# Performance work log

Hardware: AMD Instinct MI355X
Metric: run time of the kernel (lower is better)

Reference implementation:

```python
import jax, jax.numpy as jnp
import numpy as np

# --- Bark-band constants (from init_kwargs: bark_num=25, fs=32000, win_len=1024) ---
WIDTHS = np.array([3, 3, 3, 3, 4, 4, 4, 5, 5, 6, 7, 8, 9, 10, 12, 14, 18, 22, 29, 35, 42, 58, 80, 128])
NB = 24              # bark_num - 1 bands
F = 512              # win_len // 2 frequency bins (WIDTHS sums to 512)
FS = 32000
WIN = 1024
SEG = np.repeat(np.arange(NB), WIDTHS)          # [F] bin -> band id (0-based)
MASK = np.zeros((F, NB), dtype=np.float32)
MASK[np.arange(F), SEG] = 1.0                   # one-hot band membership [F, NB]
K = WIDTHS.astype(np.float32)                   # band widths k_i
# absolute threshold of hearing (tq) per bin, f = (bin+1)*fs/win_len
_f = (np.arange(F) + 1.0) * FS / WIN
TQ = (3.64 * (_f / 1000 + 1e-6) ** (-0.8)
      - 6.5 * np.exp(-0.6 * (_f / 1000 - 3.3) ** 2)
      + 1e-3 * (_f / 1000) ** 4).astype(np.float32)

B, T = 32, 1200


def setup_inputs() -> dict:
    key = jax.random.key(0)
    k1, k2, k3, k4 = jax.random.split(key, 4)
    return {
        "log_magnitude": jax.random.normal(k1, (B, T, F), dtype=jnp.float32),
        "real": jax.random.normal(k2, (B, T, F), dtype=jnp.float32),
        "imag": jax.random.normal(k3, (B, T, F), dtype=jnp.float32),
        "spread_function": jax.random.uniform(k4, (NB, NB), dtype=jnp.float32),
    }


def reference(log_magnitude, real, imag, spread_function):
    eps = 1e-8
    spec = jnp.exp(jnp.clip(log_magnitude, -1000.0, 10.0))          # [B,T,F], > 0
    dt = spec.dtype
    M = jnp.asarray(MASK, dt)
    k = jnp.asarray(K, dt)                                           # [NB]
    seg = jnp.asarray(SEG)                                           # [F]

    # per-band sums (spec > 0 so abs(spec) == spec)
    psum = spec @ M                                                  # [B,T,NB]
    logsum = jnp.log10(jnp.abs(spec) + 1e-30) @ M                    # [B,T,NB]
    geo = 10.0 ** (logsum / k)
    ari = psum / k

    sfm = 10.0 * jnp.log10(geo / ari + eps)                          # spectral flatness [B,T,NB]
    alpha = jnp.minimum(sfm / (-60.0), 1.0)
    band_idx = jnp.arange(1, NB + 1, dtype=dt)
    offset = alpha * (14.5 + band_idx) + (1.0 - alpha) * 5.5
    toff = -offset / 10.0                                            # [B,T,NB]

    c = jnp.log10(psum @ spread_function + eps)                      # [B,T,NB]
    c_test = jnp.log10(jnp.sum(spread_function, axis=0) + eps)       # [NB] (ones @ S)
    t = 10.0 ** (c + toff)
    renorm = 10.0 ** (c_test + toff)
    t = t / renorm                                                   # [B,T,NB]

    # scatter band thresholds back to bins, floor by hearing threshold
    t_bin = jnp.maximum(jnp.take(t, seg, axis=-1), jnp.asarray(TQ, dt))  # [B,T,F]
    k_bin = jnp.take(k, seg)                                         # [F]
    denom = jnp.sqrt(6.0 * t_bin / k_bin)

    rp = real * spec
    ip = imag * spec
    pe_r = jnp.log2(2.0 * jnp.abs(rp / denom) + 1.0)
    pe_i = jnp.log2(2.0 * jnp.abs(ip / denom) + 1.0)

    # original: loss = sum_i mean(pe_real_band_i) + mean(pe_imag_band_i)
    # == weighted sum with per-bin weight 1 / (B*T*k_i)
    w = 1.0 / (spec.shape[0] * spec.shape[1] * k_bin)                # [F]
    loss = jnp.sum((pe_r + pe_i) * w)
    return 1.0 / (loss + 1.0)
```

## Files before the change

### kernel.cpp

```cpp
#include <hip/hip_runtime.h>
#include <math.h>

#define NB     24
#define FBIN   512
#define ROWS   (32*1200)
#define GRID   2048
#define BLK    256
#define WPB    4
#define NWAVES (GRID*WPB)
#define SLOTS  20
#define LOG2E  1.44269504f

__device__ __constant__ int   c_off[NB+1] = {0,3,6,9,12,16,20,24,29,34,40,47,55,64,74,86,100,118,140,169,204,246,304,384,512};
__device__ __constant__ float c_k[NB]     = {3,3,3,3,4,4,4,5,5,6,7,8,9,10,12,14,18,22,29,35,42,58,80,128};

__global__ __launch_bounds__(BLK) void pe_main(const float* __restrict__ lm,
                                               const float* __restrict__ re,
                                               const float* __restrict__ im,
                                               const float* __restrict__ S,
                                               float* __restrict__ partial)
{
    __shared__ float s_slot[WPB][NB*SLOTS];

    const int tid  = threadIdx.x;
    const int w    = tid >> 6;
    const int lane = tid & 63;
    float* const slot = s_slot[w];

    for (int i = lane; i < NB*SLOTS; i += 64) slot[i] = 0.f;

    const int bin0 = lane * 8;
    int waddr[8], band4[8];
    float tq[8], a4[8];
    #pragma unroll
    for (int j = 0; j < 8; ++j) {
        const int binj = bin0 + j;
        int b = 0;
        for (int q = 0; q < NB; ++q) if (binj >= c_off[q+1]) b++;
        band4[j] = b << 2;
        waddr[j] = b*SLOTS + (lane - (c_off[b] >> 3));
        const float z = (binj + 1) * 0.03125f;
        tq[j] = 3.64f*__builtin_amdgcn_exp2f(-0.8f*__builtin_amdgcn_logf(z + 1e-6f))
              - 6.5f*__builtin_amdgcn_exp2f(-0.6f*LOG2E*(z-3.3f)*(z-3.3f))
              + 1e-3f*z*z*z*z;
        a4[j] = 1.5f / c_k[b];
    }

    const int cl = (lane < NB) ? lane : 0;
    float Sreg[NB];
    float colsum = 1e-8f;
    #pragma unroll
    for (int i = 0; i < NB; ++i) { Sreg[i] = S[i*NB + cl]; colsum += Sreg[i]; }
    const float invcol = 1.0f / colsum;

    const int gw = blockIdx.x * WPB + w;
    size_t base = (size_t)gw * FBIN + bin0;
    const size_t step = (size_t)NWAVES * FBIN;

    float4 L0 = *(const float4*)(lm + base);
    float4 L1 = *(const float4*)(lm + base + 4);

    float acc = 0.f;
    for (int row = gw; row < ROWS; row += NWAVES) {
        const float4 R0 = *(const float4*)(re + base);
        const float4 R1 = *(const float4*)(re + base + 4);
        const float4 I0 = *(const float4*)(im + base);
        const float4 I1 = *(const float4*)(im + base + 4);

        const float lmv[8] = {L0.x,L0.y,L0.z,L0.w,L1.x,L1.y,L1.z,L1.w};
        float sp[8];
        #pragma unroll
        for (int j = 0; j < 8; ++j)
            sp[j] = __builtin_amdgcn_exp2f(fminf(lmv[j], 10.f) * LOG2E);

        {
            float ps = sp[0];
            slot[waddr[0]] = ps;
            #pragma unroll
            for (int j = 1; j < 8; ++j) {
                ps = (waddr[j] == waddr[j-1]) ? ps + sp[j] : sp[j];
                slot[waddr[j]] = ps;
            }
        }

        const size_t nb = base + ((row + NWAVES < ROWS) ? step : (size_t)0);
        const float4 nL0 = *(const float4*)(lm + nb);
        const float4 nL1 = *(const float4*)(lm + nb + 4);

        asm volatile("s_waitcnt lgkmcnt(0)" ::: "memory");

        float psum_v = 0.f;
        if (lane < NB) {
            const float4* sp4 = (const float4*)(slot + lane*SLOTS);
            const float4 q0 = sp4[0], q1 = sp4[1], q2 = sp4[2], q3 = sp4[3], q4 = sp4[4];
            psum_v = ((((q0.x+q0.y)+(q0.z+q0.w)) + ((q1.x+q1.y)+(q1.z+q1.w)))
                   +  (((q2.x+q2.y)+(q2.z+q2.w)) + ((q3.x+q3.y)+(q3.z+q3.w))))
                   +   ((q4.x+q4.y)+(q4.z+q4.w));
        }

        float tmine;
        {
            float c0 = 1e-8f, c1 = 0.f, c2 = 0.f, c3 = 0.f;
            #pragma unroll
            for (int i = 0; i < NB; i += 4) {
                const float p0 = __int_as_float(__builtin_amdgcn_readlane(__float_as_int(psum_v), i+0));
                const float p1 = __int_as_float(__builtin_amdgcn_readlane(__float_as_int(psum_v), i+1));
                const float p2 = __int_as_float(__builtin_amdgcn_readlane(__float_as_int(psum_v), i+2));
                const float p3 = __int_as_float(__builtin_amdgcn_readlane(__float_as_int(psum_v), i+3));
                c0 = fmaf(p0, Sreg[i+0], c0);
                c1 = fmaf(p1, Sreg[i+1], c1);
                c2 = fmaf(p2, Sreg[i+2], c2);
                c3 = fmaf(p3, Sreg[i+3], c3);
            }
            tmine = ((c0+c1)+(c2+c3)) * invcol;
        }

        float tb[8];
        #pragma unroll
        for (int j = 0; j < 8; ++j)
            tb[j] = __int_as_float(__builtin_amdgcn_ds_bpermute(band4[j], __float_as_int(tmine)));

        const float rv[8] = {R0.x,R0.y,R0.z,R0.w,R1.x,R1.y,R1.z,R1.w};
        const float iv[8] = {I0.x,I0.y,I0.z,I0.w,I1.x,I1.y,I1.z,I1.w};
        #pragma unroll
        for (int j = 0; j < 8; ++j) {
            const float t  = fmaxf(tb[j], tq[j]);
            const float s  = __builtin_amdgcn_rsqf(a4[j] * t);
            const float u  = sp[j] * s;
            const float pr = fmaf(fabsf(rv[j]), u, 1.0f);
            const float pi = fmaf(fabsf(iv[j]), u, 1.0f);
            acc = fmaf(__builtin_amdgcn_logf(pr * pi), a4[j], acc);
        }

        asm volatile("s_waitcnt lgkmcnt(0)" ::: "memory");

        L0 = nL0; L1 = nL1;
        base += step;
    }

    #pragma unroll
    for (int o = 32; o > 0; o >>= 1) acc += __shfl_xor(acc, o, 64);
    if (lane == 0) partial[gw] = acc * (1.0f/57600.0f);
}

__global__ __launch_bounds__(256) void pe_final(const float* __restrict__ partial,
                                                float* __restrict__ out)
{
    __shared__ double sred[256];
    const int tid = threadIdx.x;
    double s = 0.0;
    for (int i = tid; i < NWAVES; i += 256) s += (double)partial[i];
    sred[tid] = s;
    __syncthreads();
    for (int k = 128; k > 0; k >>= 1) {
        if (tid < k) sred[tid] += sred[tid+k];
        __syncthreads();
    }
    if (tid == 0) out[0] = (float)(1.0 / (sred[0] + 1.0));
}

extern "C" void kernel_launch(void* const* d_in, const int* in_sizes, int n_in,
                              void* d_out, int out_size, void* d_ws, size_t ws_size,
                              hipStream_t stream) {
    const float* lm = (const float*)d_in[0];
    const float* re = (const float*)d_in[1];
    const float* im = (const float*)d_in[2];
    const float* S  = (const float*)d_in[3];
    float* partial = (float*)d_ws;
    pe_main<<<GRID, BLK, 0, stream>>>(lm, re, im, S, partial);
    pe_final<<<1, 256, 0, stream>>>(partial, (float*)d_out);
}
```

Before: 51.41 us.

## Process two rows per loop iteration with double-buffered LDS slots

The main loop now handles two rows per iteration, issuing all global loads for both rows up front and interleaving their band-sum, spreading and entropy computations to expose more independent work. The spread-function matrix moves from 24 per-lane registers into a transposed, padded LDS copy with precomputed inverse column sums, freeing registers. Slot buffers are double-buffered by parity, so the trailing LDS wait can be dropped. In exchange it loses the explicit next-row prefetch, adds LDS reads of S in the inner loop, and uses a masked duplicate row when the row count is odd.

```diff
diff --git a/kernel.cpp b/kernel.cpp
--- a/kernel.cpp
+++ b/kernel.cpp
@@ -9,10 +9,13 @@
 #define WPB    4
 #define NWAVES (GRID*WPB)
 #define SLOTS  20
+#define SCOLP  28
 #define LOG2E  1.44269504f
 
 __device__ __constant__ int   c_off[NB+1] = {0,3,6,9,12,16,20,24,29,34,40,47,55,64,74,86,100,118,140,169,204,246,304,384,512};
 __device__ __constant__ float c_k[NB]     = {3,3,3,3,4,4,4,5,5,6,7,8,9,10,12,14,18,22,29,35,42,58,80,128};
+
+#define RDLANE(v,i) __int_as_float(__builtin_amdgcn_readlane(__float_as_int(v), (i)))
 
 __global__ __launch_bounds__(BLK) void pe_main(const float* __restrict__ lm,
                                                const float* __restrict__ re,
@@ -20,14 +23,30 @@
                                                const float* __restrict__ S,
                                                float* __restrict__ partial)
 {
-    __shared__ float s_slot[WPB][NB*SLOTS];
+    __shared__ float s_slot[WPB][2][2][NB*SLOTS];
+    __shared__ float s_Scol[NB*SCOLP];
+    __shared__ float s_invc[NB];
 
     const int tid  = threadIdx.x;
     const int w    = tid >> 6;
     const int lane = tid & 63;
-    float* const slot = s_slot[w];
-
-    for (int i = lane; i < NB*SLOTS; i += 64) slot[i] = 0.f;
+
+    for (int i = tid; i < NB*NB; i += BLK) {
+        const int r = i / NB, c = i - r*NB;
+        s_Scol[c*SCOLP + r] = S[i];
+    }
+    __syncthreads();
+    if (tid < NB) {
+        float cs = 1e-8f;
+        for (int i = 0; i < NB; ++i) cs += s_Scol[tid*SCOLP + i];
+        s_invc[tid] = 1.0f / cs;
+    }
+    __syncthreads();
+
+    {
+        float* sw = &s_slot[w][0][0][0];
+        for (int i = lane; i < 2*2*NB*SLOTS; i += 64) sw[i] = 0.f;
+    }
 
     const int bin0 = lane * 8;
     int waddr[8], band4[8];
@@ -45,97 +64,114 @@
               + 1e-3f*z*z*z*z;
         a4[j] = 1.5f / c_k[b];
     }
-
-    const int cl = (lane < NB) ? lane : 0;
-    float Sreg[NB];
-    float colsum = 1e-8f;
-    #pragma unroll
-    for (int i = 0; i < NB; ++i) { Sreg[i] = S[i*NB + cl]; colsum += Sreg[i]; }
-    const float invcol = 1.0f / colsum;
+    const int cl = (lane < NB) ? lane : NB-1;
+    const float invcol = s_invc[cl];
 
     const int gw = blockIdx.x * WPB + w;
-    size_t base = (size_t)gw * FBIN + bin0;
-    const size_t step = (size_t)NWAVES * FBIN;
-
-    float4 L0 = *(const float4*)(lm + base);
-    float4 L1 = *(const float4*)(lm + base + 4);
+    const size_t rstep = (size_t)NWAVES * FBIN;
+    size_t base0 = (size_t)gw * FBIN + bin0;
 
     float acc = 0.f;
-    for (int row = gw; row < ROWS; row += NWAVES) {
-        const float4 R0 = *(const float4*)(re + base);
-        const float4 R1 = *(const float4*)(re + base + 4);
-        const float4 I0 = *(const float4*)(im + base);
-        const float4 I1 = *(const float4*)(im + base + 4);
-
-        const float lmv[8] = {L0.x,L0.y,L0.z,L0.w,L1.x,L1.y,L1.z,L1.w};
-        float sp[8];
+    int par = 0;
+    for (int r0 = gw; r0 < ROWS; r0 += 2*NWAVES) {
+        const bool  v1    = (r0 + NWAVES) < ROWS;
+        const float m1    = v1 ? 1.f : 0.f;
+        const size_t base1 = v1 ? base0 + rstep : base0;
+
+        const float4 A0 = *(const float4*)(lm + base0), A1 = *(const float4*)(lm + base0 + 4);
+        const float4 B0 = *(const float4*)(lm + base1), B1 = *(const float4*)(lm + base1 + 4);
+        const float4 Ra0 = *(const float4*)(re + base0), Ra1 = *(const float4*)(re + base0 + 4);
+        const float4 Rb0 = *(const float4*)(re + base1), Rb1 = *(const float4*)(re + base1 + 4);
+        const float4 Ia0 = *(const float4*)(im + base0), Ia1 = *(const float4*)(im + base0 + 4);
+        const float4 Ib0 = *(const float4*)(im + base1), Ib1 = *(const float4*)(im + base1 + 4);
+
+        const float la[8] = {A0.x,A0.y,A0.z,A0.w,A1.x,A1.y,A1.z,A1.w};
+        const float lb[8] = {B0.x,B0.y,B0.z,B0.w,B1.x,B1.y,B1.z,B1.w};
+        float spa[8], spb[8];
         #pragma unroll
-        for (int j = 0; j < 8; ++j)
-            sp[j] = __builtin_amdgcn_exp2f(fminf(lmv[j], 10.f) * LOG2E);
-
+        for (int j = 0; j < 8; ++j) {
+            spa[j] = __builtin_amdgcn_exp2f(fminf(la[j], 10.f) * LOG2E);
+            spb[j] = __builtin_amdgcn_exp2f(fminf(lb[j], 10.f) * LOG2E);
+        }
+
+        float* const sa = &s_slot[w][par][0][0];
+        float* const sb = &s_slot[w][par][1][0];
         {
-            float ps = sp[0];
-            slot[waddr[0]] = ps;
+            float pa = spa[0], pb = spb[0];
+            sa[waddr[0]] = pa; sb[waddr[0]] = pb;
             #pragma unroll
             for (int j = 1; j < 8; ++j) {
-                ps = (waddr[j] == waddr[j-1]) ? ps + sp[j] : sp[j];
-                slot[waddr[j]] = ps;
+                const bool same = (waddr[j] == waddr[j-1]);
+                pa = same ? pa + spa[j] : spa[j];
+                pb = same ? pb + spb[j] : spb[j];
+                sa[waddr[j]] = pa; sb[waddr[j]] = pb;
             }
         }
 
-        const size_t nb = base + ((row + NWAVES < ROWS) ? step : (size_t)0);
-        const float4 nL0 = *(const float4*)(lm + nb);
-        const float4 nL1 = *(const float4*)(lm + nb + 4);
-
         asm volatile("s_waitcnt lgkmcnt(0)" ::: "memory");
 
-        float psum_v = 0.f;
+        float psa = 0.f, psb = 0.f;
         if (lane < NB) {
-            const float4* sp4 = (const float4*)(slot + lane*SLOTS);
-            const float4 q0 = sp4[0], q1 = sp4[1], q2 = sp4[2], q3 = sp4[3], q4 = sp4[4];
-            psum_v = ((((q0.x+q0.y)+(q0.z+q0.w)) + ((q1.x+q1.y)+(q1.z+q1.w)))
-                   +  (((q2.x+q2.y)+(q2.z+q2.w)) + ((q3.x+q3.y)+(q3.z+q3.w))))
-                   +   ((q4.x+q4.y)+(q4.z+q4.w));
-        }
-
-        float tmine;
+            const float4* qa = (const float4*)(sa + lane*SLOTS);
+            const float4* qb = (const float4*)(sb + lane*SLOTS);
+            const float4 a0=qa[0],a1=qa[1],a2=qa[2],a3=qa[3],a4_=qa[4];
+            const float4 b0=qb[0],b1=qb[1],b2=qb[2],b3=qb[3],b4_=qb[4];
+            psa = ((((a0.x+a0.y)+(a0.z+a0.w)) + ((a1.x+a1.y)+(a1.z+a1.w)))
+                +  (((a2.x+a2.y)+(a2.z+a2.w)) + ((a3.x+a3.y)+(a3.z+a3.w))))
+                +   ((a4_.x+a4_.y)+(a4_.z+a4_.w));
+            psb = ((((b0.x+b0.y)+(b0.z+b0.w)) + ((b1.x+b1.y)+(b1.z+b1.w)))
+                +  (((b2.x+b2.y)+(b2.z+b2.w)) + ((b3.x+b3.y)+(b3.z+b3.w))))
+                +   ((b4_.x+b4_.y)+(b4_.z+b4_.w));
+        }
+
+        float ta, tb;
         {
-            float c0 = 1e-8f, c1 = 0.f, c2 = 0.f, c3 = 0.f;
+            const float* Sc = &s_Scol[cl*SCOLP];
+            float a0=1e-8f,a1=0.f,a2=0.f,a3=0.f, b0=1e-8f,b1=0.f,b2=0.f,b3=0.f;
             #pragma unroll
             for (int i = 0; i < NB; i += 4) {
-                const float p0 = __int_as_float(__builtin_amdgcn_readlane(__float_as_int(psum_v), i+0));
-                const float p1 = __int_as_float(__builtin_amdgcn_readlane(__float_as_int(psum_v), i+1));
-                const float p2 = __int_as_float(__builtin_amdgcn_readlane(__float_as_int(psum_v), i+2));
-                const float p3 = __int_as_float(__builtin_amdgcn_readlane(__float_as_int(psum_v), i+3));
-                c0 = fmaf(p0, Sreg[i+0], c0);
-                c1 = fmaf(p1, Sreg[i+1], c1);
-                c2 = fmaf(p2, Sreg[i+2], c2);
-                c3 = fmaf(p3, Sreg[i+3], c3);
+                const float4 q = *(const float4*)(Sc + i);
+                a0 = fmaf(RDLANE(psa,i+0), q.x, a0);  b0 = fmaf(RDLANE(psb,i+0), q.x, b0);
+                a1 = fmaf(RDLANE(psa,i+1), q.y, a1);  b1 = fmaf(RDLANE(psb,i+1), q.y, b1);
+                a2 = fmaf(RDLANE(psa,i+2), q.z, a2);  b2 = fmaf(RDLANE(psb,i+2), q.z, b2);
+                a3 = fmaf(RDLANE(psa,i+3), q.w, a3);  b3 = fmaf(RDLANE(psb,i+3), q.w, b3);
             }
-            tmine = ((c0+c1)+(c2+c3)) * invcol;
-        }
-
-        float tb[8];
-        #pragma unroll
-        for (int j = 0; j < 8; ++j)
-            tb[j] = __int_as_float(__builtin_amdgcn_ds_bpermute(band4[j], __float_as_int(tmine)));
-
-        const float rv[8] = {R0.x,R0.y,R0.z,R0.w,R1.x,R1.y,R1.z,R1.w};
-        const float iv[8] = {I0.x,I0.y,I0.z,I0.w,I1.x,I1.y,I1.z,I1.w};
+            ta = ((a0+a1)+(a2+a3)) * invcol;
+            tb = ((b0+b1)+(b2+b3)) * invcol;
+        }
+
+        float tba[8], tbb[8];
         #pragma unroll
         for (int j = 0; j < 8; ++j) {
-            const float t  = fmaxf(tb[j], tq[j]);
-            const float s  = __builtin_amdgcn_rsqf(a4[j] * t);
-            const float u  = sp[j] * s;
-            const float pr = fmaf(fabsf(rv[j]), u, 1.0f);
-            const float pi = fmaf(fabsf(iv[j]), u, 1.0f);
-            acc = fmaf(__builtin_amdgcn_logf(pr * pi), a4[j], acc);
-        }
-
-        asm volatile("s_waitcnt lgkmcnt(0)" ::: "memory");
-
-        L0 = nL0; L1 = nL1;
-        base += step;
+            tba[j] = __int_as_float(__builtin_amdgcn_ds_bpermute(band4[j], __float_as_int(ta)));
+            tbb[j] = __int_as_float(__builtin_amdgcn_ds_bpermute(band4[j], __float_as_int(tb)));
+        }
+
+        const float rva[8] = {Ra0.x,Ra0.y,Ra0.z,Ra0.w,Ra1.x,Ra1.y,Ra1.z,Ra1.w};
+        const float iva[8] = {Ia0.x,Ia0.y,Ia0.z,Ia0.w,Ia1.x,Ia1.y,Ia1.z,Ia1.w};
+        const float rvb[8] = {Rb0.x,Rb0.y,Rb0.z,Rb0.w,Rb1.x,Rb1.y,Rb1.z,Rb1.w};
+        const float ivb[8] = {Ib0.x,Ib0.y,Ib0.z,Ib0.w,Ib1.x,Ib1.y,Ib1.z,Ib1.w};
+        float accB = 0.f;
+        #pragma unroll
+        for (int j = 0; j < 8; ++j) {
+            const float t0 = fmaxf(tba[j], tq[j]);
+            const float s0 = __builtin_amdgcn_rsqf(a4[j] * t0);
+            const float u0 = spa[j] * s0;
+            const float pr0 = fmaf(fabsf(rva[j]), u0, 1.0f);
+            const float pi0 = fmaf(fabsf(iva[j]), u0, 1.0f);
+            acc  = fmaf(__builtin_amdgcn_logf(pr0 * pi0), a4[j], acc);
+
+            const float t1 = fmaxf(tbb[j], tq[j]);
+            const float s1 = __builtin_amdgcn_rsqf(a4[j] * t1);
+            const float u1 = spb[j] * s1;
+            const float pr1 = fmaf(fabsf(rvb[j]), u1, 1.0f);
+            const float pi1 = fmaf(fabsf(ivb[j]), u1, 1.0f);
+            accB = fmaf(__builtin_amdgcn_logf(pr1 * pi1), a4[j], accB);
+        }
+        acc = fmaf(accB, m1, acc);
+
+        par ^= 1;
+        base0 += 2*rstep;
     }
 
     #pragma unroll
```

New measurement: 57.24 us. 1.11x slower.

## Cut register pressure: S in LDS, packed band indices, double-buffered slots

Applied to the files above, without the earlier changes.

Moves the spread-function column out of 24 per-lane registers into a padded, transposed LDS table read as float4. Band indices for bpermute are packed into two 32-bit words and the segment-continuation test becomes a precomputed bitmask. Launch bounds now request 8 waves per SIMD. The per-wave slot buffer is double-buffered by iteration parity, which removes the trailing lgkmcnt wait, and the re/im loads are moved after the LDS wait. The aim is higher occupancy and better latency hiding, at the cost of extra LDS reads and block-level syncs in the prologue.

```diff
diff --git a/kernel.cpp b/kernel.cpp
--- a/kernel.cpp
+++ b/kernel.cpp
@@ -9,49 +9,68 @@
 #define WPB    4
 #define NWAVES (GRID*WPB)
 #define SLOTS  20
+#define SCOLP  28
 #define LOG2E  1.44269504f
 
 __device__ __constant__ int   c_off[NB+1] = {0,3,6,9,12,16,20,24,29,34,40,47,55,64,74,86,100,118,140,169,204,246,304,384,512};
 __device__ __constant__ float c_k[NB]     = {3,3,3,3,4,4,4,5,5,6,7,8,9,10,12,14,18,22,29,35,42,58,80,128};
 
-__global__ __launch_bounds__(BLK) void pe_main(const float* __restrict__ lm,
-                                               const float* __restrict__ re,
-                                               const float* __restrict__ im,
-                                               const float* __restrict__ S,
-                                               float* __restrict__ partial)
+#define RDLANE(v,i) __int_as_float(__builtin_amdgcn_readlane(__float_as_int(v), (i)))
+
+__global__ __launch_bounds__(BLK, 8) void pe_main(const float* __restrict__ lm,
+                                                  const float* __restrict__ re,
+                                                  const float* __restrict__ im,
+                                                  const float* __restrict__ S,
+                                                  float* __restrict__ partial)
 {
-    __shared__ float s_slot[WPB][NB*SLOTS];
+    __shared__ float s_slot[WPB][2][NB*SLOTS];
+    __shared__ float s_Scol[NB*SCOLP];
+    __shared__ float s_invc[NB];
 
     const int tid  = threadIdx.x;
     const int w    = tid >> 6;
     const int lane = tid & 63;
-    float* const slot = s_slot[w];
 
-    for (int i = lane; i < NB*SLOTS; i += 64) slot[i] = 0.f;
+    for (int i = tid; i < NB*NB; i += BLK) {
+        const int r = i / NB, c = i - r*NB;
+        s_Scol[c*SCOLP + r] = S[i];
+    }
+    __syncthreads();
+    if (tid < NB) {
+        float cs = 1e-8f;
+        for (int i = 0; i < NB; ++i) cs += s_Scol[tid*SCOLP + i];
+        s_invc[tid] = 1.0f / cs;
+    }
+    __syncthreads();
+
+    {
+        float* sw = &s_slot[w][0][0];
+        for (int i = lane; i < 2*NB*SLOTS; i += 64) sw[i] = 0.f;
+    }
 
     const int bin0 = lane * 8;
-    int waddr[8], band4[8];
+    int waddr[8];
+    unsigned bpk0 = 0, bpk1 = 0;
+    unsigned smask = 0;
     float tq[8], a4[8];
     #pragma unroll
     for (int j = 0; j < 8; ++j) {
         const int binj = bin0 + j;
         int b = 0;
         for (int q = 0; q < NB; ++q) if (binj >= c_off[q+1]) b++;
-        band4[j] = b << 2;
+        if (j < 4) bpk0 |= (unsigned)(b << 2) << (8*j);
+        else       bpk1 |= (unsigned)(b << 2) << (8*(j-4));
         waddr[j] = b*SLOTS + (lane - (c_off[b] >> 3));
+        if (j > 0 && waddr[j] == waddr[j-1]) smask |= 1u << j;
         const float z = (binj + 1) * 0.03125f;
         tq[j] = 3.64f*__builtin_amdgcn_exp2f(-0.8f*__builtin_amdgcn_logf(z + 1e-6f))
               - 6.5f*__builtin_amdgcn_exp2f(-0.6f*LOG2E*(z-3.3f)*(z-3.3f))
               + 1e-3f*z*z*z*z;
         a4[j] = 1.5f / c_k[b];
     }
-
-    const int cl = (lane < NB) ? lane : 0;
-    float Sreg[NB];
-    float colsum = 1e-8f;
-    #pragma unroll
-    for (int i = 0; i < NB; ++i) { Sreg[i] = S[i*NB + cl]; colsum += Sreg[i]; }
-    const float invcol = 1.0f / colsum;
+    const int cl = (lane < NB) ? lane : NB-1;
+    const float invcol = s_invc[cl];
+    const float* const Sc = &s_Scol[cl*SCOLP];
 
     const int gw = blockIdx.x * WPB + w;
     size_t base = (size_t)gw * FBIN + bin0;
@@ -61,24 +80,21 @@
     float4 L1 = *(const float4*)(lm + base + 4);
 
     float acc = 0.f;
+    int par = 0;
     for (int row = gw; row < ROWS; row += NWAVES) {
-        const float4 R0 = *(const float4*)(re + base);
-        const float4 R1 = *(const float4*)(re + base + 4);
-        const float4 I0 = *(const float4*)(im + base);
-        const float4 I1 = *(const float4*)(im + base + 4);
-
         const float lmv[8] = {L0.x,L0.y,L0.z,L0.w,L1.x,L1.y,L1.z,L1.w};
         float sp[8];
         #pragma unroll
         for (int j = 0; j < 8; ++j)
             sp[j] = __builtin_amdgcn_exp2f(fminf(lmv[j], 10.f) * LOG2E);
 
+        float* const slot = &s_slot[w][par][0];
         {
             float ps = sp[0];
             slot[waddr[0]] = ps;
             #pragma unroll
             for (int j = 1; j < 8; ++j) {
-                ps = (waddr[j] == waddr[j-1]) ? ps + sp[j] : sp[j];
+                ps = ((smask >> j) & 1u) ? ps + sp[j] : sp[j];
                 slot[waddr[j]] = ps;
             }
         }
@@ -89,10 +105,15 @@
 
         asm volatile("s_waitcnt lgkmcnt(0)" ::: "memory");
 
+        const float4 R0 = *(const float4*)(re + base);
+        const float4 R1 = *(const float4*)(re + base + 4);
+        const float4 I0 = *(const float4*)(im + base);
+        const float4 I1 = *(const float4*)(im + base + 4);
+
         float psum_v = 0.f;
         if (lane < NB) {
-            const float4* sp4 = (const float4*)(slot + lane*SLOTS);
-            const float4 q0 = sp4[0], q1 = sp4[1], q2 = sp4[2], q3 = sp4[3], q4 = sp4[4];
+            const float4* q = (const float4*)(slot + lane*SLOTS);
+            const float4 q0=q[0], q1=q[1], q2=q[2], q3=q[3], q4=q[4];
             psum_v = ((((q0.x+q0.y)+(q0.z+q0.w)) + ((q1.x+q1.y)+(q1.z+q1.w)))
                    +  (((q2.x+q2.y)+(q2.z+q2.w)) + ((q3.x+q3.y)+(q3.z+q3.w))))
                    +   ((q4.x+q4.y)+(q4.z+q4.w));
@@ -103,22 +124,22 @@
             float c0 = 1e-8f, c1 = 0.f, c2 = 0.f, c3 = 0.f;
             #pragma unroll
             for (int i = 0; i < NB; i += 4) {
-                const float p0 = __int_as_float(__builtin_amdgcn_readlane(__float_as_int(psum_v), i+0));
-                const float p1 = __int_as_float(__builtin_amdgcn_readlane(__float_as_int(psum_v), i+1));
-                const float p2 = __int_as_float(__builtin_amdgcn_readlane(__float_as_int(psum_v), i+2));
-                const float p3 = __int_as_float(__builtin_amdgcn_readlane(__float_as_int(psum_v), i+3));
-                c0 = fmaf(p0, Sreg[i+0], c0);
-                c1 = fmaf(p1, Sreg[i+1], c1);
-                c2 = fmaf(p2, Sreg[i+2], c2);
-                c3 = fmaf(p3, Sreg[i+3], c3);
+                const float4 q = *(const float4*)(Sc + i);
+                c0 = fmaf(RDLANE(psum_v,i+0), q.x, c0);
+                c1 = fmaf(RDLANE(psum_v,i+1), q.y, c1);
+                c2 = fmaf(RDLANE(psum_v,i+2), q.z, c2);
+                c3 = fmaf(RDLANE(psum_v,i+3), q.w, c3);
             }
             tmine = ((c0+c1)+(c2+c3)) * invcol;
         }
 
         float tb[8];
         #pragma unroll
-        for (int j = 0; j < 8; ++j)
-            tb[j] = __int_as_float(__builtin_amdgcn_ds_bpermute(band4[j], __float_as_int(tmine)));
+        for (int j = 0; j < 8; ++j) {
+            const unsigned pk = (j < 4) ? bpk0 : bpk1;
+            const int b4 = (int)((pk >> (8*(j & 3))) & 0xffu);
+            tb[j] = __int_as_float(__builtin_amdgcn_ds_bpermute(b4, __float_as_int(tmine)));
+        }
 
         const float rv[8] = {R0.x,R0.y,R0.z,R0.w,R1.x,R1.y,R1.z,R1.w};
         const float iv[8] = {I0.x,I0.y,I0.z,I0.w,I1.x,I1.y,I1.z,I1.w};
@@ -132,8 +153,7 @@
             acc = fmaf(__builtin_amdgcn_logf(pr * pi), a4[j], acc);
         }
 
-        asm volatile("s_waitcnt lgkmcnt(0)" ::: "memory");
-
+        par ^= 1;
         L0 = nL0; L1 = nL1;
         base += step;
     }
```

Result: slower. 155.6 us (+202.7%).

## Prefetch re/im rows, double-buffer LDS slots, hoist per-bin rsqrt to band level

Applied to the files above, without the earlier changes.

Loads of real and imag for the next row are now issued in the same iteration as the log-magnitude prefetch, so all three input streams are software-pipelined one row ahead. The per-wave LDS slot buffer is double-buffered by parity, which lets the trailing lgkmcnt wait at the end of each iteration be dropped. The rsqrt of the band threshold is moved from 8 per-lane evaluations to one per band lane, combined with a precomputed rsqrt of the hearing threshold through fminf. That identity relies on rsqrt being monotone with positive thresholds. The cost is more live registers for the prefetched float4s, which may reduce occupancy.

```diff
diff --git a/kernel.cpp b/kernel.cpp
--- a/kernel.cpp
+++ b/kernel.cpp
@@ -14,24 +14,29 @@
 __device__ __constant__ int   c_off[NB+1] = {0,3,6,9,12,16,20,24,29,34,40,47,55,64,74,86,100,118,140,169,204,246,304,384,512};
 __device__ __constant__ float c_k[NB]     = {3,3,3,3,4,4,4,5,5,6,7,8,9,10,12,14,18,22,29,35,42,58,80,128};
 
+#define RDLANE(v,i) __int_as_float(__builtin_amdgcn_readlane(__float_as_int(v), (i)))
+
 __global__ __launch_bounds__(BLK) void pe_main(const float* __restrict__ lm,
                                                const float* __restrict__ re,
                                                const float* __restrict__ im,
                                                const float* __restrict__ S,
                                                float* __restrict__ partial)
 {
-    __shared__ float s_slot[WPB][NB*SLOTS];
+    __shared__ float s_slot[WPB][2][NB*SLOTS];
 
     const int tid  = threadIdx.x;
     const int w    = tid >> 6;
     const int lane = tid & 63;
-    float* const slot = s_slot[w];
 
-    for (int i = lane; i < NB*SLOTS; i += 64) slot[i] = 0.f;
+    {
+        float* sw = &s_slot[w][0][0];
+        for (int i = lane; i < 2*NB*SLOTS; i += 64) sw[i] = 0.f;
+    }
 
     const int bin0 = lane * 8;
     int waddr[8], band4[8];
-    float tq[8], a4[8];
+    unsigned smask = 0;
+    float rtq[8], a4[8];
     #pragma unroll
     for (int j = 0; j < 8; ++j) {
         const int binj = bin0 + j;
@@ -39,102 +44,98 @@
         for (int q = 0; q < NB; ++q) if (binj >= c_off[q+1]) b++;
         band4[j] = b << 2;
         waddr[j] = b*SLOTS + (lane - (c_off[b] >> 3));
+        if (j > 0 && waddr[j] == waddr[j-1]) smask |= 1u << j;
         const float z = (binj + 1) * 0.03125f;
-        tq[j] = 3.64f*__builtin_amdgcn_exp2f(-0.8f*__builtin_amdgcn_logf(z + 1e-6f))
-              - 6.5f*__builtin_amdgcn_exp2f(-0.6f*LOG2E*(z-3.3f)*(z-3.3f))
-              + 1e-3f*z*z*z*z;
+        const float tqj = 3.64f*__builtin_amdgcn_exp2f(-0.8f*__builtin_amdgcn_logf(z + 1e-6f))
+                        - 6.5f*__builtin_amdgcn_exp2f(-0.6f*LOG2E*(z-3.3f)*(z-3.3f))
+                        + 1e-3f*z*z*z*z;
         a4[j] = 1.5f / c_k[b];
+        rtq[j] = (tqj > 0.f) ? __builtin_amdgcn_rsqf(a4[j] * tqj) : 3.4e38f;
     }
 
-    const int cl = (lane < NB) ? lane : 0;
+    const int cl = (lane < NB) ? lane : NB-1;
     float Sreg[NB];
     float colsum = 1e-8f;
     #pragma unroll
     for (int i = 0; i < NB; ++i) { Sreg[i] = S[i*NB + cl]; colsum += Sreg[i]; }
-    const float invcol = 1.0f / colsum;
+    const float invcol  = 1.0f / colsum;
+    const float abandcl = 1.5f / c_k[cl];
 
     const int gw = blockIdx.x * WPB + w;
     size_t base = (size_t)gw * FBIN + bin0;
     const size_t step = (size_t)NWAVES * FBIN;
 
-    float4 L0 = *(const float4*)(lm + base);
-    float4 L1 = *(const float4*)(lm + base + 4);
+    float4 L0 = *(const float4*)(lm + base), L1 = *(const float4*)(lm + base + 4);
+    float4 R0 = *(const float4*)(re + base), R1 = *(const float4*)(re + base + 4);
+    float4 I0 = *(const float4*)(im + base), I1 = *(const float4*)(im + base + 4);
 
     float acc = 0.f;
+    int par = 0;
     for (int row = gw; row < ROWS; row += NWAVES) {
-        const float4 R0 = *(const float4*)(re + base);
-        const float4 R1 = *(const float4*)(re + base + 4);
-        const float4 I0 = *(const float4*)(im + base);
-        const float4 I1 = *(const float4*)(im + base + 4);
-
         const float lmv[8] = {L0.x,L0.y,L0.z,L0.w,L1.x,L1.y,L1.z,L1.w};
         float sp[8];
         #pragma unroll
         for (int j = 0; j < 8; ++j)
             sp[j] = __builtin_amdgcn_exp2f(fminf(lmv[j], 10.f) * LOG2E);
 
+        float* const slot = &s_slot[w][par][0];
         {
             float ps = sp[0];
             slot[waddr[0]] = ps;
             #pragma unroll
             for (int j = 1; j < 8; ++j) {
-                ps = (waddr[j] == waddr[j-1]) ? ps + sp[j] : sp[j];
+                ps = ((smask >> j) & 1u) ? ps + sp[j] : sp[j];
                 slot[waddr[j]] = ps;
             }
         }
 
         const size_t nb = base + ((row + NWAVES < ROWS) ? step : (size_t)0);
-        const float4 nL0 = *(const float4*)(lm + nb);
-        const float4 nL1 = *(const float4*)(lm + nb + 4);
+        const float4 nL0 = *(const float4*)(lm + nb), nL1 = *(const float4*)(lm + nb + 4);
+        const float4 nR0 = *(const float4*)(re + nb), nR1 = *(const float4*)(re + nb + 4);
+        const float4 nI0 = *(const float4*)(im + nb), nI1 = *(const float4*)(im + nb + 4);
 
         asm volatile("s_waitcnt lgkmcnt(0)" ::: "memory");
 
         float psum_v = 0.f;
         if (lane < NB) {
-            const float4* sp4 = (const float4*)(slot + lane*SLOTS);
-            const float4 q0 = sp4[0], q1 = sp4[1], q2 = sp4[2], q3 = sp4[3], q4 = sp4[4];
+            const float4* q = (const float4*)(slot + lane*SLOTS);
+            const float4 q0=q[0], q1=q[1], q2=q[2], q3=q[3], q4=q[4];
             psum_v = ((((q0.x+q0.y)+(q0.z+q0.w)) + ((q1.x+q1.y)+(q1.z+q1.w)))
                    +  (((q2.x+q2.y)+(q2.z+q2.w)) + ((q3.x+q3.y)+(q3.z+q3.w))))
                    +   ((q4.x+q4.y)+(q4.z+q4.w));
         }
 
-        float tmine;
+        float vb;
         {
             float c0 = 1e-8f, c1 = 0.f, c2 = 0.f, c3 = 0.f;
             #pragma unroll
             for (int i = 0; i < NB; i += 4) {
-                const float p0 = __int_as_float(__builtin_amdgcn_readlane(__float_as_int(psum_v), i+0));
-                const float p1 = __int_as_float(__builtin_amdgcn_readlane(__float_as_int(psum_v), i+1));
-                const float p2 = __int_as_float(__builtin_amdgcn_readlane(__float_as_int(psum_v), i+2));
-                const float p3 = __int_as_float(__builtin_amdgcn_readlane(__float_as_int(psum_v), i+3));
-                c0 = fmaf(p0, Sreg[i+0], c0);
-                c1 = fmaf(p1, Sreg[i+1], c1);
-                c2 = fmaf(p2, Sreg[i+2], c2);
-                c3 = fmaf(p3, Sreg[i+3], c3);
+                c0 = fmaf(RDLANE(psum_v,i+0), Sreg[i+0], c0);
+                c1 = fmaf(RDLANE(psum_v,i+1), Sreg[i+1], c1);
+                c2 = fmaf(RDLANE(psum_v,i+2), Sreg[i+2], c2);
+                c3 = fmaf(RDLANE(psum_v,i+3), Sreg[i+3], c3);
             }
-            tmine = ((c0+c1)+(c2+c3)) * invcol;
+            const float tmine = ((c0+c1)+(c2+c3)) * invcol;
+            vb = __builtin_amdgcn_rsqf(abandcl * tmine);
         }
 
-        float tb[8];
+        float vbb[8];
         #pragma unroll
         for (int j = 0; j < 8; ++j)
-            tb[j] = __int_as_float(__builtin_amdgcn_ds_bpermute(band4[j], __float_as_int(tmine)));
+            vbb[j] = __int_as_float(__builtin_amdgcn_ds_bpermute(band4[j], __float_as_int(vb)));
 
         const float rv[8] = {R0.x,R0.y,R0.z,R0.w,R1.x,R1.y,R1.z,R1.w};
         const float iv[8] = {I0.x,I0.y,I0.z,I0.w,I1.x,I1.y,I1.z,I1.w};
         #pragma unroll
         for (int j = 0; j < 8; ++j) {
-            const float t  = fmaxf(tb[j], tq[j]);
-            const float s  = __builtin_amdgcn_rsqf(a4[j] * t);
-            const float u  = sp[j] * s;
+            const float u  = sp[j] * fminf(vbb[j], rtq[j]);
             const float pr = fmaf(fabsf(rv[j]), u, 1.0f);
             const float pi = fmaf(fabsf(iv[j]), u, 1.0f);
             acc = fmaf(__builtin_amdgcn_logf(pr * pi), a4[j], acc);
         }
 
-        asm volatile("s_waitcnt lgkmcnt(0)" ::: "memory");
-
-        L0 = nL0; L1 = nL1;
+        par ^= 1;
+        L0 = nL0; L1 = nL1; R0 = nR0; R1 = nR1; I0 = nI0; I1 = nI1;
         base += step;
     }
 
```

Result: no change. 51.78 us (+0.7%).
